# Kernel optimization log

Hardware: AMD Instinct MI355X
Metric: run time of the kernel (lower is better)

## Reference

```python
import jax, jax.numpy as jnp
import numpy as np

N, F, C, H, E, NC = 100000, 128, 64, 4, 1600000, 2
BN_EPS = 1e-5


def _bn(x, g, b):
    mu = x.mean(0)
    var = x.var(0)  # biased variance, as torch BN uses for normalization
    return (x - mu) / jnp.sqrt(var + BN_EPS) * g + b


def _gat(x, src, dst, W, a_src, a_dst, bias, heads, out_ch, concat, n):
    # x:[n,in] -> h:[n,heads,out_ch]
    h = (x @ W).reshape(n, heads, out_ch)
    e_src = (h * a_src[None]).sum(-1)  # [n,heads]
    e_dst = (h * a_dst[None]).sum(-1)
    logits = jax.nn.leaky_relu(e_src[src] + e_dst[dst], 0.2)  # [e,heads]
    m = jax.ops.segment_max(logits, dst, num_segments=n)
    m = jnp.where(jnp.isfinite(m), m, 0.0)
    ex = jnp.exp(logits - m[dst])
    denom = jax.ops.segment_sum(ex, dst, num_segments=n)
    alpha = ex / denom[dst]  # segment softmax over incoming edges
    out = jax.ops.segment_sum(alpha[:, :, None] * h[src], dst, num_segments=n)
    out = out.reshape(n, heads * out_ch) if concat else out.mean(axis=1)
    return out + bias


def _sage(x, src, dst, Wl, bl, Wr, n):
    agg = jax.ops.segment_sum(x[src], dst, num_segments=n)
    cnt = jax.ops.segment_sum(jnp.ones_like(src, dtype=x.dtype), dst, num_segments=n)
    agg = agg / jnp.maximum(cnt, 1.0)[:, None]  # mean aggregation
    return agg @ Wl + bl + x @ Wr


def setup_inputs() -> dict:
    key = jax.random.key(0)
    ks = jax.random.split(key, 24)
    def rn(k, shape, fan):
        return jax.random.normal(k, shape, jnp.float32) * (1.0 / np.sqrt(fan))
    inp = {}
    inp['x'] = jax.random.normal(ks[0], (N, F), jnp.float32)
    inp['edge_index'] = jax.random.randint(ks[1], (2, E), 0, N, jnp.int32)
    # GAT layer 1: in=F, out=C, heads=H, concat
    inp['W1g'] = rn(ks[2], (F, H * C), F)
    inp['a_src1'] = rn(ks[3], (H, C), C)
    inp['a_dst1'] = rn(ks[4], (H, C), C)
    inp['b1g'] = jnp.zeros((H * C,), jnp.float32)
    inp['bn1g_g'] = jnp.ones((H * C,), jnp.float32)
    inp['bn1g_b'] = jnp.zeros((H * C,), jnp.float32)
    # GAT layer 2: in=H*C, out=C, heads=1, no concat
    inp['W2g'] = rn(ks[5], (H * C, C), H * C)
    inp['a_src2'] = rn(ks[6], (1, C), C)
    inp['a_dst2'] = rn(ks[7], (1, C), C)
    inp['b2g'] = jnp.zeros((C,), jnp.float32)
    # SAGE layer 1
    inp['Wl1'] = rn(ks[8], (F, C), F)
    inp['bl1'] = jnp.zeros((C,), jnp.float32)
    inp['Wr1'] = rn(ks[9], (F, C), F)
    inp['bn1s_g'] = jnp.ones((C,), jnp.float32)
    inp['bn1s_b'] = jnp.zeros((C,), jnp.float32)
    # SAGE layer 2
    inp['Wl2'] = rn(ks[10], (C, C), C)
    inp['bl2'] = jnp.zeros((C,), jnp.float32)
    inp['Wr2'] = rn(ks[11], (C, C), C)
    # fusion MLP
    inp['Wf1'] = rn(ks[12], (2 * C, C), 2 * C)
    inp['bf1'] = jnp.zeros((C,), jnp.float32)
    inp['Wf2'] = rn(ks[13], (C, NC), C)
    inp['bf2'] = jnp.zeros((NC,), jnp.float32)
    return inp


def reference(x, edge_index, W1g, a_src1, a_dst1, b1g, bn1g_g, bn1g_b,
              W2g, a_src2, a_dst2, b2g, Wl1, bl1, Wr1, bn1s_g, bn1s_b,
              Wl2, bl2, Wr2, Wf1, bf1, Wf2, bf2):
    n = x.shape[0]
    src, dst = edge_index[0], edge_index[1]
    # PyG GATConv adds self-loops by default
    loop = jnp.arange(n, dtype=src.dtype)
    src_l = jnp.concatenate([src, loop])
    dst_l = jnp.concatenate([dst, loop])

    # GAT branch (dropout = identity in eval)
    g = _gat(x, src_l, dst_l, W1g, a_src1, a_dst1, b1g, H, C, True, n)
    g = jax.nn.elu(_bn(g, bn1g_g, bn1g_b))
    g = _gat(g, src_l, dst_l, W2g, a_src2, a_dst2, b2g, 1, C, False, n)

    # SAGE branch (no self-loops in SAGEConv)
    s = _sage(x, src, dst, Wl1, bl1, Wr1, n)
    s = jax.nn.relu(_bn(s, bn1s_g, bn1s_b))
    s = _sage(s, src, dst, Wl2, bl2, Wr2, n)

    h = jnp.concatenate([g, s], axis=-1)  # [n, 2C]
    h = jax.nn.relu(h @ Wf1 + bf1)
    return h @ Wf2 + bf2  # logits [n, NC]
```

## Files before the change

kernel.cpp:

```cpp
#include <hip/hip_runtime.h>
#include <math.h>


typedef unsigned short u16;
typedef u16 us4 __attribute__((ext_vector_type(4)));
typedef short s8v __attribute__((ext_vector_type(8)));
typedef float f4v __attribute__((ext_vector_type(4)));

__device__ __forceinline__ float b2f(u16 u) {
  union { unsigned int i; float f; } v; v.i = ((unsigned int)u) << 16; return v.f;
}
__device__ __forceinline__ u16 f2b(float f) {
  union { float f; unsigned int i; } v; v.f = f;
  unsigned int u = v.i;
  return (u16)((u + 0x7fffu + ((u >> 16) & 1u)) >> 16);
}

__global__ __launch_bounds__(256) void k_cast(const float* __restrict__ s, u16* __restrict__ d, int n4) {
  int i = blockIdx.x * blockDim.x + threadIdx.x;
  if (i < n4) {
    float4 v = *(reinterpret_cast<const float4*>(s) + i);
    us4 o = { f2b(v.x), f2b(v.y), f2b(v.z), f2b(v.w) };
    *(reinterpret_cast<us4*>(d) + i) = o;
  }
}

struct WcastDesc { const float* W; u16* Wt; int K; int M; };
struct WcastAll { WcastDesc d[5]; };
__global__ __launch_bounds__(256) void k_wcast_all(WcastAll a) {
  WcastDesc de = a.d[blockIdx.y];
  int n = de.K * de.M;
  int idx = blockIdx.x * blockDim.x + threadIdx.x;
  if (idx >= n) return;
  int c = idx / de.K, k = idx - c * de.K;
  de.Wt[idx] = f2b(de.W[(size_t)k * de.M + c]);
}

__global__ __launch_bounds__(256) void k_combine(const float* __restrict__ Wl2, const float* __restrict__ Wr2,
                                                 const float* __restrict__ bl2, const float* __restrict__ Wf1,
                                                 const float* __restrict__ bf1, u16* __restrict__ Wc1t,
                                                 u16* __restrict__ Wc2t, float* __restrict__ biasC) {
  int idx = blockIdx.x * 256 + threadIdx.x;
  if (idx >= 4096) return;
  int m = idx >> 6, k = idx & 63;
  float s1 = 0.f, s2 = 0.f;
  for (int j = 0; j < 64; ++j) {
    float wf = Wf1[(size_t)(64 + j) * 64 + m];
    s1 += Wl2[k * 64 + j] * wf;
    s2 += Wr2[k * 64 + j] * wf;
  }
  Wc1t[m * 64 + k] = f2b(s1);
  Wc2t[m * 64 + k] = f2b(s2);
  if (k == 0) {
    float b = bf1[m];
    for (int j = 0; j < 64; ++j) b += bl2[j] * Wf1[(size_t)(64 + j) * 64 + m];
    biasC[m] = b;
  }
}

__global__ __launch_bounds__(256) void k_deg(const int* __restrict__ ei, int* __restrict__ deg, int E) {
  int e = blockIdx.x * blockDim.x + threadIdx.x;
  if (e < E) atomicAdd(&deg[ei[E + e]], 1);
}

__global__ __launch_bounds__(256) void k_scan1(const int* __restrict__ deg, int* __restrict__ row_ptr,
                                               int* __restrict__ bsum, int n) {
  __shared__ int sh[256];
  int tid = threadIdx.x;
  int i = blockIdx.x * 256 + tid;
  int v = (i < n) ? deg[i] : 0;
  sh[tid] = v;
  __syncthreads();
  for (int off = 1; off < 256; off <<= 1) {
    int t = (tid >= off) ? sh[tid - off] : 0;
    __syncthreads();
    sh[tid] += t;
    __syncthreads();
  }
  if (i < n) row_ptr[i] = sh[tid] - v;
  if (tid == 255) bsum[blockIdx.x] = sh[255];
}

__global__ __launch_bounds__(1024) void k_scan2(int* __restrict__ bsum, int* __restrict__ total, int nb) {
  __shared__ int sh[1024];
  int tid = threadIdx.x;
  int v = (tid < nb) ? bsum[tid] : 0;
  sh[tid] = v;
  __syncthreads();
  for (int off = 1; off < 1024; off <<= 1) {
    int t = (tid >= off) ? sh[tid - off] : 0;
    __syncthreads();
    sh[tid] += t;
    __syncthreads();
  }
  if (tid < nb) bsum[tid] = sh[tid] - v;
  if (tid == 1023) *total = sh[1023];
}

__global__ __launch_bounds__(256) void k_scan3(int* __restrict__ row_ptr, const int* __restrict__ bsum, int n) {
  int i = blockIdx.x * 256 + threadIdx.x;
  if (i < n) row_ptr[i] += bsum[blockIdx.x];
}

__global__ __launch_bounds__(256) void k_scatter(const int* __restrict__ ei, const int* __restrict__ row_ptr,
                                                 int* __restrict__ cursor, int* __restrict__ csr_src, int E) {
  int e = blockIdx.x * blockDim.x + threadIdx.x;
  if (e < E) {
    int d = ei[E + e];
    int pos = row_ptr[d] + atomicAdd(&cursor[d], 1);
    csr_src[pos] = ei[e];
  }
}

struct Seg { const u16* Wt; u16* out; int ldout; const float* bias; int head; };
struct Segs6 { Seg s[6]; };
__global__ __launch_bounds__(256) void k_gemm_multi(const u16* __restrict__ A, Segs6 sg,
                                                    const float* __restrict__ a_src1, const float* __restrict__ a_dst1,
                                                    float* __restrict__ es1, float* __restrict__ ed1, int Nrows) {
  Seg seg = sg.s[blockIdx.y];
  __shared__ u16 As[64][40];
  __shared__ u16 Bs[64][40];
  int row0 = blockIdx.x * 64;
  int tid = threadIdx.x;
  int w = tid >> 6, lane = tid & 63;
  int lr = tid >> 2;
  int lseg = (tid & 3) * 8;
  f4v acc[4];
#pragma unroll
  for (int nn = 0; nn < 4; ++nn) acc[nn] = (f4v){0.f, 0.f, 0.f, 0.f};
  int ar = (w << 4) + (lane & 15);
  int ak = (lane >> 4) << 3;

  for (int k0 = 0; k0 < 128; k0 += 32) {
    __syncthreads();
    int gr = row0 + lr;
    s8v av = {};
    if (gr < Nrows) av = *reinterpret_cast<const s8v*>(A + (size_t)gr * 128 + k0 + lseg);
    *reinterpret_cast<s8v*>(&As[lr][lseg]) = av;
    s8v bv = *reinterpret_cast<const s8v*>(seg.Wt + (size_t)lr * 128 + k0 + lseg);
    *reinterpret_cast<s8v*>(&Bs[lr][lseg]) = bv;
    __syncthreads();
    s8v af = *reinterpret_cast<const s8v*>(&As[ar][ak]);
#pragma unroll
    for (int nn = 0; nn < 4; ++nn) {
      s8v bf = *reinterpret_cast<const s8v*>(&Bs[(nn << 4) + (lane & 15)][ak]);
      acc[nn] = __builtin_amdgcn_mfma_f32_16x16x32_bf16(af, bf, acc[nn], 0, 0, 0);
    }
  }
  int r0 = row0 + (w << 4) + ((lane >> 4) << 2);
  int cc = lane & 15;
#pragma unroll
  for (int nn = 0; nn < 4; ++nn) {
    int gc = (nn << 4) + cc;
    float bv = seg.bias ? seg.bias[gc] : 0.f;
#pragma unroll
    for (int j = 0; j < 4; ++j) {
      int gr = r0 + j;
      if (gr < Nrows) seg.out[(size_t)gr * seg.ldout + gc] = f2b(acc[nn][j] + bv);
    }
  }
  if (seg.head >= 0) {
    int s = seg.head;
    float pe[4] = {0.f, 0.f, 0.f, 0.f}, pd[4] = {0.f, 0.f, 0.f, 0.f};
#pragma unroll
    for (int nn = 0; nn < 4; ++nn) {
      int col = (nn << 4) + cc;
      float asv = a_src1[s * 64 + col];
      float adv = a_dst1[s * 64 + col];
#pragma unroll
      for (int j = 0; j < 4; ++j) {
        pe[j] += acc[nn][j] * asv;
        pd[j] += acc[nn][j] * adv;
      }
    }
#pragma unroll
    for (int off = 1; off < 16; off <<= 1) {
#pragma unroll
      for (int j = 0; j < 4; ++j) {
        pe[j] += __shfl_xor(pe[j], off, 64);
        pd[j] += __shfl_xor(pd[j], off, 64);
      }
    }
    if (cc == 0) {
#pragma unroll
      for (int j = 0; j < 4; ++j) {
        int gr = r0 + j;
        if (gr < Nrows) {
          es1[(size_t)gr * 4 + s] = pe[j];
          ed1[(size_t)gr * 4 + s] = pd[j];
        }
      }
    }
  }
}

__global__ __launch_bounds__(256) void k_gemm_bn(const u16* __restrict__ A, const u16* __restrict__ Wt,
                                                 const float* __restrict__ sc, const float* __restrict__ sh,
                                                 const float* __restrict__ a_src2, const float* __restrict__ a_dst2,
                                                 u16* __restrict__ C, float* __restrict__ es2,
                                                 float* __restrict__ ed2, int Nrows) {
  __shared__ u16 As[64][40];
  __shared__ u16 Bs[64][40];
  int row0 = blockIdx.x * 64;
  int tid = threadIdx.x;
  int w = tid >> 6, lane = tid & 63;
  int lr = tid >> 2;
  int lseg = (tid & 3) * 8;
  f4v acc[4];
#pragma unroll
  for (int nn = 0; nn < 4; ++nn) acc[nn] = (f4v){0.f, 0.f, 0.f, 0.f};
  int ar = (w << 4) + (lane & 15);
  int ak = (lane >> 4) << 3;

  for (int k0 = 0; k0 < 256; k0 += 32) {
    __syncthreads();
    int gr = row0 + lr;
    s8v av = {};
    if (gr < Nrows) {
      av = *reinterpret_cast<const s8v*>(A + (size_t)gr * 256 + k0 + lseg);
#pragma unroll
      for (int j = 0; j < 8; ++j) {
        int c = k0 + lseg + j;
        float a = b2f((u16)av[j]) * sc[c] + sh[c];
        a = (a > 0.f) ? a : (__expf(a) - 1.f);
        av[j] = (short)f2b(a);
      }
    }
    *reinterpret_cast<s8v*>(&As[lr][lseg]) = av;
    s8v bv = *reinterpret_cast<const s8v*>(Wt + (size_t)lr * 256 + k0 + lseg);
    *reinterpret_cast<s8v*>(&Bs[lr][lseg]) = bv;
    __syncthreads();
    s8v af = *reinterpret_cast<const s8v*>(&As[ar][ak]);
#pragma unroll
    for (int nn = 0; nn < 4; ++nn) {
      s8v bf = *reinterpret_cast<const s8v*>(&Bs[(nn << 4) + (lane & 15)][ak]);
      acc[nn] = __builtin_amdgcn_mfma_f32_16x16x32_bf16(af, bf, acc[nn], 0, 0, 0);
    }
  }
  int r0 = row0 + (w << 4) + ((lane >> 4) << 2);
  int cc = lane & 15;
  float pe[4] = {0.f, 0.f, 0.f, 0.f}, pd[4] = {0.f, 0.f, 0.f, 0.f};
#pragma unroll
  for (int nn = 0; nn < 4; ++nn) {
    int gc = (nn << 4) + cc;
    float asv = a_src2[gc], adv = a_dst2[gc];
#pragma unroll
    for (int j = 0; j < 4; ++j) {
      float hv = acc[nn][j];
      pe[j] += hv * asv;
      pd[j] += hv * adv;
      int gr = r0 + j;
      if (gr < Nrows) C[(size_t)gr * 64 + gc] = f2b(hv);
    }
  }
#pragma unroll
  for (int off = 1; off < 16; off <<= 1) {
#pragma unroll
    for (int j = 0; j < 4; ++j) {
      pe[j] += __shfl_xor(pe[j], off, 64);
      pd[j] += __shfl_xor(pd[j], off, 64);
    }
  }
  if (cc == 0) {
#pragma unroll
    for (int j = 0; j < 4; ++j) {
      int gr = r0 + j;
      if (gr < Nrows) { es2[gr] = pe[j]; ed2[gr] = pd[j]; }
    }
  }
}

__global__ __launch_bounds__(256) void k_gat_stats4(const float* __restrict__ es, const float* __restrict__ ed,
                                                    const int* __restrict__ row_ptr, const int* __restrict__ csr,
                                                    float* __restrict__ alphaE, float* __restrict__ alphaS, int n) {
  int wid = (blockIdx.x * blockDim.x + threadIdx.x) >> 6;
  int lane = threadIdx.x & 63;
  if (wid >= n) return;
  int start = row_ptr[wid];
  int deg = row_ptr[wid + 1] - start;
  int h = lane & 3, esl = lane >> 2;
  float edst = ed[(size_t)wid * 4 + h];

  float m = -1e30f, s = 0.f;
  for (int e = esl; e < deg + 1; e += 16) {
    int sn = (e < deg) ? csr[start + e] : wid;
    float v = es[(size_t)sn * 4 + h] + edst;
    v = (v >= 0.f) ? v : 0.2f * v;
    if (v > m) { s = s * __expf(m - v) + 1.f; m = v; }
    else s += __expf(v - m);
  }
#pragma unroll
  for (int off = 4; off < 64; off <<= 1) {
    float mo = __shfl_xor(m, off, 64);
    float so = __shfl_xor(s, off, 64);
    float M = fmaxf(m, mo);
    s = s * __expf(m - M) + so * __expf(mo - M);
    m = M;
  }
  float invS = 1.f / s;
  for (int e = esl; e < deg + 1; e += 16) {
    int sn = (e < deg) ? csr[start + e] : wid;
    float v = es[(size_t)sn * 4 + h] + edst;
    v = (v >= 0.f) ? v : 0.2f * v;
    float a = __expf(v - m) * invS;
    if (e < deg) alphaE[(size_t)(start + e) * 4 + h] = a;
    else alphaS[(size_t)wid * 4 + h] = a;
  }
}

__global__ __launch_bounds__(256) void k_gat_stats1(const float* __restrict__ es, const float* __restrict__ ed,
                                                    const int* __restrict__ row_ptr, const int* __restrict__ csr,
                                                    float* __restrict__ alphaE, float* __restrict__ alphaS, int n) {
  int wid = (blockIdx.x * blockDim.x + threadIdx.x) >> 6;
  int lane = threadIdx.x & 63;
  if (wid >= n) return;
  int start = row_ptr[wid];
  int deg = row_ptr[wid + 1] - start;
  float edst = ed[wid];
  float m = -1e30f, s = 0.f;
  for (int e = lane; e < deg + 1; e += 64) {
    int sn = (e < deg) ? csr[start + e] : wid;
    float v = es[sn] + edst;
    v = (v >= 0.f) ? v : 0.2f * v;
    if (v > m) { s = s * __expf(m - v) + 1.f; m = v; }
    else s += __expf(v - m);
  }
#pragma unroll
  for (int off = 1; off < 64; off <<= 1) {
    float mo = __shfl_xor(m, off, 64);
    float so = __shfl_xor(s, off, 64);
    float M = fmaxf(m, mo);
    s = s * __expf(m - M) + so * __expf(mo - M);
    m = M;
  }
  float invS = 1.f / s;
  for (int e = lane; e < deg + 1; e += 64) {
    int sn = (e < deg) ? csr[start + e] : wid;
    float v = es[sn] + edst;
    v = (v >= 0.f) ? v : 0.2f * v;
    float a = __expf(v - m) * invS;
    if (e < deg) alphaE[start + e] = a;
    else alphaS[wid] = a;
  }
}

template <int H, int C>
__global__ __launch_bounds__(256) void k_gat_agg2(const u16* __restrict__ h, const float* __restrict__ alphaE,
                                                  const float* __restrict__ alphaS, const int* __restrict__ row_ptr,
                                                  const int* __restrict__ csr, const float* __restrict__ bias,
                                                  u16* __restrict__ out, int n) {
  constexpr int HC = H * C;
  constexpr int VW = HC / 64;
  int wid = (blockIdx.x * blockDim.x + threadIdx.x) >> 6;
  int lane = threadIdx.x & 63;
  if (wid >= n) return;
  int start = row_ptr[wid];
  int deg = row_ptr[wid + 1] - start;
  int hl = (lane * VW) / C;

  float acc[VW];
  {
    float aS = alphaS[(size_t)wid * H + hl];
    if constexpr (VW == 4) {
      us4 hv = *(reinterpret_cast<const us4*>(h + (size_t)wid * HC) + lane);
#pragma unroll
      for (int j = 0; j < 4; ++j) acc[j] = aS * b2f(hv[j]);
    } else {
      acc[0] = aS * b2f(h[(size_t)wid * HC + lane]);
    }
  }

  int e = 0;
  for (; e + 4 <= deg; e += 4) {
    int sn[4];
    float al[4];
#pragma unroll
    for (int i = 0; i < 4; ++i) {
      sn[i] = csr[start + e + i];
      al[i] = alphaE[(size_t)(start + e + i) * H + hl];
    }
#pragma unroll
    for (int i = 0; i < 4; ++i) {
      if constexpr (VW == 4) {
        us4 hv = *(reinterpret_cast<const us4*>(h + (size_t)sn[i] * HC) + lane);
#pragma unroll
        for (int j = 0; j < 4; ++j) acc[j] += al[i] * b2f(hv[j]);
      } else {
        acc[0] += al[i] * b2f(h[(size_t)sn[i] * HC + lane]);
      }
    }
  }
  for (; e < deg; ++e) {
    int sn = csr[start + e];
    float al = alphaE[(size_t)(start + e) * H + hl];
    if constexpr (VW == 4) {
      us4 hv = *(reinterpret_cast<const us4*>(h + (size_t)sn * HC) + lane);
#pragma unroll
      for (int j = 0; j < 4; ++j) acc[j] += al * b2f(hv[j]);
    } else {
      acc[0] += al * b2f(h[(size_t)sn * HC + lane]);
    }
  }

  int c0 = lane * VW;
#pragma unroll
  for (int j = 0; j < VW; ++j) out[(size_t)wid * HC + c0 + j] = f2b(acc[j] + bias[c0 + j]);
}

__global__ __launch_bounds__(256) void k_sage_agg64(const u16* __restrict__ x, const int* __restrict__ row_ptr,
                                                    const int* __restrict__ csr, const u16* __restrict__ Cin,
                                                    const float* __restrict__ sc, const float* __restrict__ sh,
                                                    u16* __restrict__ agg, int n) {
  int wid = (blockIdx.x * blockDim.x + threadIdx.x) >> 6;
  int lane = threadIdx.x & 63;
  if (wid >= n) return;
  int start = row_ptr[wid];
  int deg = row_ptr[wid + 1] - start;
  bool bn = sc != nullptr;
  float scv = 1.f, shv = 0.f;
  if (bn) { scv = sc[lane]; shv = sh[lane]; }
  float acc = 0.f;
  int e = 0;
  for (; e + 4 <= deg; e += 4) {
    int sn[4];
#pragma unroll
    for (int i = 0; i < 4; ++i) sn[i] = csr[start + e + i];
#pragma unroll
    for (int i = 0; i < 4; ++i) {
      float v = b2f(x[(size_t)sn[i] * 64 + lane]);
      if (bn) v = fmaxf(v * scv + shv, 0.f);
      acc += v;
    }
  }
  for (; e < deg; ++e) {
    float v = b2f(x[(size_t)csr[start + e] * 64 + lane]);
    if (bn) v = fmaxf(v * scv + shv, 0.f);
    acc += v;
  }
  float inv = 1.f / fmaxf((float)deg, 1.f);
  float base = Cin ? b2f(Cin[(size_t)wid * 64 + lane]) : 0.f;
  agg[(size_t)wid * 64 + lane] = f2b(acc * inv + base);
}

template <int CH>
__global__ __launch_bounds__(256) void k_bn_stats(const u16* __restrict__ x, float* __restrict__ stats, int n) {
  constexpr int RPB = 256 / CH;
  int tid = threadIdx.x;
  int c = tid % CH;
  int rsub = tid / CH;
  float s = 0.f, q = 0.f;
  for (int r = blockIdx.x * RPB + rsub; r < n; r += gridDim.x * RPB) {
    float v = b2f(x[(size_t)r * CH + c]);
    s += v;
    q += v * v;
  }
  __shared__ float ls[256], lq[256];
  ls[tid] = s; lq[tid] = q;
  __syncthreads();
  if (tid < CH) {
#pragma unroll
    for (int i = 1; i < RPB; ++i) { s += ls[tid + i * CH]; q += lq[tid + i * CH]; }
    atomicAdd(&stats[c], s);
    atomicAdd(&stats[CH + c], q);
  }
}

__global__ __launch_bounds__(256) void k_bn_final2(const float* __restrict__ statsG, const float* __restrict__ statsS,
                                                   const float* __restrict__ gG, const float* __restrict__ bG,
                                                   const float* __restrict__ gS, const float* __restrict__ bS,
                                                   float* __restrict__ scG, float* __restrict__ shG,
                                                   float* __restrict__ scS, float* __restrict__ shS, int n) {
  int c = threadIdx.x;
  float invn = 1.f / (float)n;
  {
    float mu = statsG[c] * invn;
    float var = statsG[256 + c] * invn - mu * mu;
    float rs = rsqrtf(var + 1e-5f) * gG[c];
    scG[c] = rs;
    shG[c] = bG[c] - mu * rs;
  }
  if (c < 64) {
    float mu = statsS[c] * invn;
    float var = statsS[64 + c] * invn - mu * mu;
    float rs = rsqrtf(var + 1e-5f) * gS[c];
    scS[c] = rs;
    shS[c] = bS[c] - mu * rs;
  }
}

__global__ __launch_bounds__(256) void k_gemm_final(const u16* __restrict__ A1, const u16* __restrict__ W1,
                                                    const u16* __restrict__ A2, const u16* __restrict__ W2,
                                                    const u16* __restrict__ A3, const u16* __restrict__ W3,
                                                    const float* __restrict__ scS, const float* __restrict__ shS,
                                                    const float* __restrict__ biasC, const float* __restrict__ Wf2,
                                                    const float* __restrict__ bf2, float* __restrict__ out,
                                                    int Nrows) {
  __shared__ u16 As[64][40];
  __shared__ u16 Bs[64][40];
  int row0 = blockIdx.x * 64;
  int tid = threadIdx.x;
  int w = tid >> 6, lane = tid & 63;
  int lr = tid >> 2;
  int lseg = (tid & 3) * 8;
  f4v acc[4];
#pragma unroll
  for (int nn = 0; nn < 4; ++nn) acc[nn] = (f4v){0.f, 0.f, 0.f, 0.f};
  int ar = (w << 4) + (lane & 15);
  int ak = (lane >> 4) << 3;

  const u16* Aarr[3] = {A1, A2, A3};
  const u16* Warr[3] = {W1, W2, W3};
#pragma unroll
  for (int ph = 0; ph < 3; ++ph) {
    const u16* A = Aarr[ph];
    const u16* Wt = Warr[ph];
#pragma unroll
    for (int k0 = 0; k0 < 64; k0 += 32) {
      __syncthreads();
      int gr = row0 + lr;
      s8v av = {};
      if (gr < Nrows) {
        av = *reinterpret_cast<const s8v*>(A + (size_t)gr * 64 + k0 + lseg);
        if (ph == 2) {
#pragma unroll
          for (int j = 0; j < 8; ++j) {
            int c = k0 + lseg + j;
            float a = fmaxf(b2f((u16)av[j]) * scS[c] + shS[c], 0.f);
            av[j] = (short)f2b(a);
          }
        }
      }
      *reinterpret_cast<s8v*>(&As[lr][lseg]) = av;
      s8v bv = *reinterpret_cast<const s8v*>(Wt + (size_t)lr * 64 + k0 + lseg);
      *reinterpret_cast<s8v*>(&Bs[lr][lseg]) = bv;
      __syncthreads();
      s8v af = *reinterpret_cast<const s8v*>(&As[ar][ak]);
#pragma unroll
      for (int nn = 0; nn < 4; ++nn) {
        s8v bf = *reinterpret_cast<const s8v*>(&Bs[(nn << 4) + (lane & 15)][ak]);
        acc[nn] = __builtin_amdgcn_mfma_f32_16x16x32_bf16(af, bf, acc[nn], 0, 0, 0);
      }
    }
  }

  int r0 = row0 + (w << 4) + ((lane >> 4) << 2);
  int cc = lane & 15;
  float p0[4] = {0.f, 0.f, 0.f, 0.f}, p1[4] = {0.f, 0.f, 0.f, 0.f};
#pragma unroll
  for (int nn = 0; nn < 4; ++nn) {
    int col = (nn << 4) + cc;
    float bC = biasC[col];
    float w0 = Wf2[col * 2 + 0], w1 = Wf2[col * 2 + 1];
#pragma unroll
    for (int j = 0; j < 4; ++j) {
      float f = fmaxf(acc[nn][j] + bC, 0.f);
      p0[j] += f * w0;
      p1[j] += f * w1;
    }
  }
#pragma unroll
  for (int off = 1; off < 16; off <<= 1) {
#pragma unroll
    for (int j = 0; j < 4; ++j) {
      p0[j] += __shfl_xor(p0[j], off, 64);
      p1[j] += __shfl_xor(p1[j], off, 64);
    }
  }
  if (cc == 0) {
    float b0 = bf2[0], b1 = bf2[1];
#pragma unroll
    for (int j = 0; j < 4; ++j) {
      int gr = r0 + j;
      if (gr < Nrows) {
        out[(size_t)gr * 2 + 0] = p0[j] + b0;
        out[(size_t)gr * 2 + 1] = p1[j] + b1;
      }
    }
  }
}

extern "C" void kernel_launch(void* const* d_in, const int* in_sizes, int n_in,
                              void* d_out, int out_size, void* d_ws, size_t ws_size,
                              hipStream_t stream) {
  const float* x      = (const float*)d_in[0];
  const int*   ei     = (const int*)d_in[1];
  const float* W1g    = (const float*)d_in[2];
  const float* a_src1 = (const float*)d_in[3];
  const float* a_dst1 = (const float*)d_in[4];
  const float* b1g    = (const float*)d_in[5];
  const float* bn1g_g = (const float*)d_in[6];
  const float* bn1g_b = (const float*)d_in[7];
  const float* W2g    = (const float*)d_in[8];
  const float* a_src2 = (const float*)d_in[9];
  const float* a_dst2 = (const float*)d_in[10];
  const float* b2g    = (const float*)d_in[11];
  const float* Wl1    = (const float*)d_in[12];
  const float* bl1    = (const float*)d_in[13];
  const float* Wr1    = (const float*)d_in[14];
  const float* bn1s_g = (const float*)d_in[15];
  const float* bn1s_b = (const float*)d_in[16];
  const float* Wl2    = (const float*)d_in[17];
  const float* bl2    = (const float*)d_in[18];
  const float* Wr2    = (const float*)d_in[19];
  const float* Wf1    = (const float*)d_in[20];
  const float* bf1    = (const float*)d_in[21];
  const float* Wf2    = (const float*)d_in[22];
  const float* bf2    = (const float*)d_in[23];

  const int N = in_sizes[0] / 128;
  const int E = in_sizes[1] / 2;

  char* ws = (char*)d_ws;
  size_t off = 0;
  auto alloc = [&](size_t bytes) -> void* {
    size_t o = (off + 255) & ~(size_t)255;
    off = o + bytes;
    return (void*)(ws + o);
  };

  u16* xb    = (u16*)alloc((size_t)N * 128 * 2);
  u16* h1b   = (u16*)alloc((size_t)N * 256 * 2);
  u16* gb    = (u16*)alloc((size_t)N * 256 * 2);
  u16* h2b   = (u16*)alloc((size_t)N * 64 * 2);
  u16* g2b   = (u16*)alloc((size_t)N * 64 * 2);
  u16* xlb   = (u16*)alloc((size_t)N * 64 * 2);
  u16* xrb   = (u16*)alloc((size_t)N * 64 * 2);
  u16* s1b   = (u16*)alloc((size_t)N * 64 * 2);
  float* es1 = (float*)alloc((size_t)N * 4 * 4);
  float* ed1 = (float*)alloc((size_t)N * 4 * 4);
  float* es2 = (float*)alloc((size_t)N * 4);
  float* ed2 = (float*)alloc((size_t)N * 4);
  float* alphaE = (float*)alloc((size_t)E * 4 * 4);
  float* alphaS = (float*)alloc((size_t)N * 4 * 4);
  int* deg     = (int*)alloc((size_t)N * 2 * 4);
  int* cursor  = deg + N;
  int* row_ptr = (int*)alloc((size_t)(N + 1) * 4);
  int* bsum    = (int*)alloc(1024 * 4);
  int* csr     = (int*)alloc((size_t)E * 4);
  float* statsG = (float*)alloc((512 + 128) * 4);
  float* statsS = statsG + 512;
  float* scg   = (float*)alloc(256 * 4);
  float* shg   = (float*)alloc(256 * 4);
  float* scs   = (float*)alloc(64 * 4);
  float* shs   = (float*)alloc(64 * 4);
  float* biasC = (float*)alloc(64 * 4);
  u16* W1t  = (u16*)alloc(256 * 128 * 2);
  u16* W2t  = (u16*)alloc(64 * 256 * 2);
  u16* Wl1t = (u16*)alloc(64 * 128 * 2);
  u16* Wr1t = (u16*)alloc(64 * 128 * 2);
  u16* Wf1at= (u16*)alloc(64 * 64 * 2);
  u16* Wc1t = (u16*)alloc(64 * 64 * 2);
  u16* Wc2t = (u16*)alloc(64 * 64 * 2);
  u16* sagg2b = h1b;

  const int tb = 256;
  const int nwb = (N + 3) / 4;
  const int nsb = (N + 255) / 256;
  const int gx = (N + 63) / 64;

  hipMemsetAsync(deg, 0, (size_t)N * 2 * 4, stream);
  hipMemsetAsync(statsG, 0, (512 + 128) * 4, stream);
  k_deg<<<(E + tb - 1) / tb, tb, 0, stream>>>(ei, deg, E);
  k_scan1<<<nsb, 256, 0, stream>>>(deg, row_ptr, bsum, N);
  k_scan2<<<1, 1024, 0, stream>>>(bsum, row_ptr + N, nsb);
  k_scan3<<<nsb, 256, 0, stream>>>(row_ptr, bsum, N);
  k_scatter<<<(E + tb - 1) / tb, tb, 0, stream>>>(ei, row_ptr, cursor, csr, E);

  k_cast<<<((N * 128 / 4) + tb - 1) / tb, tb, 0, stream>>>(x, xb, N * 128 / 4);
  WcastAll wa;
  wa.d[0] = { W1g, W1t, 128, 256 };
  wa.d[1] = { W2g, W2t, 256, 64 };
  wa.d[2] = { Wl1, Wl1t, 128, 64 };
  wa.d[3] = { Wr1, Wr1t, 128, 64 };
  wa.d[4] = { Wf1, Wf1at, 64, 64 };
  dim3 wgrid((128 * 256 + tb - 1) / tb, 5);
  k_wcast_all<<<wgrid, tb, 0, stream>>>(wa);
  k_combine<<<16, 256, 0, stream>>>(Wl2, Wr2, bl2, Wf1, bf1, Wc1t, Wc2t, biasC);

  Segs6 sg;
  sg.s[0] = { W1t,             h1b + 0,   256, nullptr, 0 };
  sg.s[1] = { W1t + 64 * 128,  h1b + 64,  256, nullptr, 1 };
  sg.s[2] = { W1t + 128 * 128, h1b + 128, 256, nullptr, 2 };
  sg.s[3] = { W1t + 192 * 128, h1b + 192, 256, nullptr, 3 };
  sg.s[4] = { Wl1t,            xlb, 64, nullptr, -1 };
  sg.s[5] = { Wr1t,            xrb, 64, bl1,     -1 };
  k_gemm_multi<<<dim3(gx, 6), 256, 0, stream>>>(xb, sg, a_src1, a_dst1, es1, ed1, N);

  k_gat_stats4<<<nwb, 256, 0, stream>>>(es1, ed1, row_ptr, csr, alphaE, alphaS, N);
  k_gat_agg2<4, 64><<<nwb, 256, 0, stream>>>(h1b, alphaE, alphaS, row_ptr, csr, b1g, gb, N);
  k_bn_stats<256><<<256, 256, 0, stream>>>(gb, statsG, N);

  k_sage_agg64<<<nwb, 256, 0, stream>>>(xlb, row_ptr, csr, xrb, nullptr, nullptr, s1b, N);
  k_bn_stats<64><<<256, 256, 0, stream>>>(s1b, statsS, N);
  k_bn_final2<<<1, 256, 0, stream>>>(statsG, statsS, bn1g_g, bn1g_b, bn1s_g, bn1s_b,
                                     scg, shg, scs, shs, N);

  k_gemm_bn<<<gx, 256, 0, stream>>>(gb, W2t, scg, shg, a_src2, a_dst2, h2b, es2, ed2, N);
  k_gat_stats1<<<nwb, 256, 0, stream>>>(es2, ed2, row_ptr, csr, alphaE, alphaS, N);
  k_gat_agg2<1, 64><<<nwb, 256, 0, stream>>>(h2b, alphaE, alphaS, row_ptr, csr, b2g, g2b, N);

  k_sage_agg64<<<nwb, 256, 0, stream>>>(s1b, row_ptr, csr, nullptr, scs, shs, sagg2b, N);

  k_gemm_final<<<gx, 256, 0, stream>>>(g2b, Wf1at, sagg2b, Wc1t, s1b, Wc2t,
                                       scs, shs, biasC, Wf2, bf2, (float*)d_out, N);
}
```

Before: 798.4 us.

## Fuse GAT and SAGE aggregations, BN stats, weight prep, and input cast

Merges the GAT and SAGE neighbour aggregations of each layer into one kernel, so the CSR indices and row pointers are read once per node for both branches. Merges the two BN statistics kernels into one launch and the weight-cast and weight-combine kernels into one. Drops the separate bf16 cast of x: the first GEMM now reads fp32 x and converts it while loading. This cuts kernel launches and the extra traffic of the cast buffer, at the cost of more registers per aggregation kernel and the GEMM re-reading fp32 x once for each of its 6 column segments.

```diff
diff --git a/kernel.cpp b/kernel.cpp
--- a/kernel.cpp
+++ b/kernel.cpp
@@ -16,45 +16,38 @@
   return (u16)((u + 0x7fffu + ((u >> 16) & 1u)) >> 16);
 }
 
-__global__ __launch_bounds__(256) void k_cast(const float* __restrict__ s, u16* __restrict__ d, int n4) {
-  int i = blockIdx.x * blockDim.x + threadIdx.x;
-  if (i < n4) {
-    float4 v = *(reinterpret_cast<const float4*>(s) + i);
-    us4 o = { f2b(v.x), f2b(v.y), f2b(v.z), f2b(v.w) };
-    *(reinterpret_cast<us4*>(d) + i) = o;
-  }
-}
-
 struct WcastDesc { const float* W; u16* Wt; int K; int M; };
-struct WcastAll { WcastDesc d[5]; };
-__global__ __launch_bounds__(256) void k_wcast_all(WcastAll a) {
-  WcastDesc de = a.d[blockIdx.y];
-  int n = de.K * de.M;
-  int idx = blockIdx.x * blockDim.x + threadIdx.x;
-  if (idx >= n) return;
-  int c = idx / de.K, k = idx - c * de.K;
-  de.Wt[idx] = f2b(de.W[(size_t)k * de.M + c]);
-}
-
-__global__ __launch_bounds__(256) void k_combine(const float* __restrict__ Wl2, const float* __restrict__ Wr2,
-                                                 const float* __restrict__ bl2, const float* __restrict__ Wf1,
-                                                 const float* __restrict__ bf1, u16* __restrict__ Wc1t,
-                                                 u16* __restrict__ Wc2t, float* __restrict__ biasC) {
+struct WPrep {
+  WcastDesc d[5];
+  const float *Wl2, *Wr2, *bl2, *Wf1, *bf1;
+  u16 *Wc1t, *Wc2t;
+  float* biasC;
+};
+__global__ __launch_bounds__(256) void k_wprep(WPrep a) {
+  int y = blockIdx.y;
   int idx = blockIdx.x * 256 + threadIdx.x;
-  if (idx >= 4096) return;
-  int m = idx >> 6, k = idx & 63;
-  float s1 = 0.f, s2 = 0.f;
-  for (int j = 0; j < 64; ++j) {
-    float wf = Wf1[(size_t)(64 + j) * 64 + m];
-    s1 += Wl2[k * 64 + j] * wf;
-    s2 += Wr2[k * 64 + j] * wf;
-  }
-  Wc1t[m * 64 + k] = f2b(s1);
-  Wc2t[m * 64 + k] = f2b(s2);
-  if (k == 0) {
-    float b = bf1[m];
-    for (int j = 0; j < 64; ++j) b += bl2[j] * Wf1[(size_t)(64 + j) * 64 + m];
-    biasC[m] = b;
+  if (y < 5) {
+    WcastDesc de = a.d[y];
+    int n = de.K * de.M;
+    if (idx >= n) return;
+    int c = idx / de.K, k = idx - c * de.K;
+    de.Wt[idx] = f2b(de.W[(size_t)k * de.M + c]);
+  } else {
+    if (idx >= 4096) return;
+    int m = idx >> 6, k = idx & 63;
+    float s1 = 0.f, s2 = 0.f;
+    for (int j = 0; j < 64; ++j) {
+      float wf = a.Wf1[(size_t)(64 + j) * 64 + m];
+      s1 += a.Wl2[k * 64 + j] * wf;
+      s2 += a.Wr2[k * 64 + j] * wf;
+    }
+    a.Wc1t[m * 64 + k] = f2b(s1);
+    a.Wc2t[m * 64 + k] = f2b(s2);
+    if (k == 0) {
+      float b = a.bf1[m];
+      for (int j = 0; j < 64; ++j) b += a.bl2[j] * a.Wf1[(size_t)(64 + j) * 64 + m];
+      a.biasC[m] = b;
+    }
   }
 }
 
@@ -114,7 +107,7 @@
 
 struct Seg { const u16* Wt; u16* out; int ldout; const float* bias; int head; };
 struct Segs6 { Seg s[6]; };
-__global__ __launch_bounds__(256) void k_gemm_multi(const u16* __restrict__ A, Segs6 sg,
+__global__ __launch_bounds__(256) void k_gemm_multi(const float* __restrict__ X, Segs6 sg,
                                                     const float* __restrict__ a_src1, const float* __restrict__ a_dst1,
                                                     float* __restrict__ es1, float* __restrict__ ed1, int Nrows) {
   Seg seg = sg.s[blockIdx.y];
@@ -135,7 +128,12 @@
     __syncthreads();
     int gr = row0 + lr;
     s8v av = {};
-    if (gr < Nrows) av = *reinterpret_cast<const s8v*>(A + (size_t)gr * 128 + k0 + lseg);
+    if (gr < Nrows) {
+      float4 lo = *reinterpret_cast<const float4*>(X + (size_t)gr * 128 + k0 + lseg);
+      float4 hi = *reinterpret_cast<const float4*>(X + (size_t)gr * 128 + k0 + lseg + 4);
+      av[0] = (short)f2b(lo.x); av[1] = (short)f2b(lo.y); av[2] = (short)f2b(lo.z); av[3] = (short)f2b(lo.w);
+      av[4] = (short)f2b(hi.x); av[5] = (short)f2b(hi.y); av[6] = (short)f2b(hi.z); av[7] = (short)f2b(hi.w);
+    }
     *reinterpret_cast<s8v*>(&As[lr][lseg]) = av;
     s8v bv = *reinterpret_cast<const s8v*>(seg.Wt + (size_t)lr * 128 + k0 + lseg);
     *reinterpret_cast<s8v*>(&Bs[lr][lseg]) = bv;
@@ -344,30 +342,25 @@
   }
 }
 
-template <int H, int C>
-__global__ __launch_bounds__(256) void k_gat_agg2(const u16* __restrict__ h, const float* __restrict__ alphaE,
-                                                  const float* __restrict__ alphaS, const int* __restrict__ row_ptr,
-                                                  const int* __restrict__ csr, const float* __restrict__ bias,
-                                                  u16* __restrict__ out, int n) {
-  constexpr int HC = H * C;
-  constexpr int VW = HC / 64;
+__global__ __launch_bounds__(256) void k_agg_gs1(const u16* __restrict__ h1, const u16* __restrict__ xl,
+                                                 const u16* __restrict__ xr, const float* __restrict__ alphaE,
+                                                 const float* __restrict__ alphaS, const int* __restrict__ row_ptr,
+                                                 const int* __restrict__ csr, const float* __restrict__ b1g,
+                                                 u16* __restrict__ gb, u16* __restrict__ s1, int n) {
   int wid = (blockIdx.x * blockDim.x + threadIdx.x) >> 6;
   int lane = threadIdx.x & 63;
   if (wid >= n) return;
   int start = row_ptr[wid];
   int deg = row_ptr[wid + 1] - start;
-  int hl = (lane * VW) / C;
-
-  float acc[VW];
+  int hl = lane >> 4;
+
+  float accG[4];
+  float accS = 0.f;
   {
-    float aS = alphaS[(size_t)wid * H + hl];
-    if constexpr (VW == 4) {
-      us4 hv = *(reinterpret_cast<const us4*>(h + (size_t)wid * HC) + lane);
-#pragma unroll
-      for (int j = 0; j < 4; ++j) acc[j] = aS * b2f(hv[j]);
-    } else {
-      acc[0] = aS * b2f(h[(size_t)wid * HC + lane]);
-    }
+    float aS = alphaS[(size_t)wid * 4 + hl];
+    us4 hv = *(reinterpret_cast<const us4*>(h1 + (size_t)wid * 256) + lane);
+#pragma unroll
+    for (int j = 0; j < 4; ++j) accG[j] = aS * b2f(hv[j]);
   }
 
   int e = 0;
@@ -377,91 +370,106 @@
 #pragma unroll
     for (int i = 0; i < 4; ++i) {
       sn[i] = csr[start + e + i];
-      al[i] = alphaE[(size_t)(start + e + i) * H + hl];
+      al[i] = alphaE[(size_t)(start + e + i) * 4 + hl];
     }
 #pragma unroll
     for (int i = 0; i < 4; ++i) {
-      if constexpr (VW == 4) {
-        us4 hv = *(reinterpret_cast<const us4*>(h + (size_t)sn[i] * HC) + lane);
-#pragma unroll
-        for (int j = 0; j < 4; ++j) acc[j] += al[i] * b2f(hv[j]);
-      } else {
-        acc[0] += al[i] * b2f(h[(size_t)sn[i] * HC + lane]);
-      }
+      us4 hv = *(reinterpret_cast<const us4*>(h1 + (size_t)sn[i] * 256) + lane);
+#pragma unroll
+      for (int j = 0; j < 4; ++j) accG[j] += al[i] * b2f(hv[j]);
+      accS += b2f(xl[(size_t)sn[i] * 64 + lane]);
     }
   }
   for (; e < deg; ++e) {
     int sn = csr[start + e];
-    float al = alphaE[(size_t)(start + e) * H + hl];
-    if constexpr (VW == 4) {
-      us4 hv = *(reinterpret_cast<const us4*>(h + (size_t)sn * HC) + lane);
-#pragma unroll
-      for (int j = 0; j < 4; ++j) acc[j] += al * b2f(hv[j]);
-    } else {
-      acc[0] += al * b2f(h[(size_t)sn * HC + lane]);
-    }
-  }
-
-  int c0 = lane * VW;
-#pragma unroll
-  for (int j = 0; j < VW; ++j) out[(size_t)wid * HC + c0 + j] = f2b(acc[j] + bias[c0 + j]);
-}
-
-__global__ __launch_bounds__(256) void k_sage_agg64(const u16* __restrict__ x, const int* __restrict__ row_ptr,
-                                                    const int* __restrict__ csr, const u16* __restrict__ Cin,
-                                                    const float* __restrict__ sc, const float* __restrict__ sh,
-                                                    u16* __restrict__ agg, int n) {
+    float al = alphaE[(size_t)(start + e) * 4 + hl];
+    us4 hv = *(reinterpret_cast<const us4*>(h1 + (size_t)sn * 256) + lane);
+#pragma unroll
+    for (int j = 0; j < 4; ++j) accG[j] += al * b2f(hv[j]);
+    accS += b2f(xl[(size_t)sn * 64 + lane]);
+  }
+
+  int c0 = lane * 4;
+#pragma unroll
+  for (int j = 0; j < 4; ++j) gb[(size_t)wid * 256 + c0 + j] = f2b(accG[j] + b1g[c0 + j]);
+  float inv = 1.f / fmaxf((float)deg, 1.f);
+  s1[(size_t)wid * 64 + lane] = f2b(accS * inv + b2f(xr[(size_t)wid * 64 + lane]));
+}
+
+__global__ __launch_bounds__(256) void k_agg_gs2(const u16* __restrict__ h2, const u16* __restrict__ s1,
+                                                 const float* __restrict__ alphaE, const float* __restrict__ alphaS,
+                                                 const int* __restrict__ row_ptr, const int* __restrict__ csr,
+                                                 const float* __restrict__ b2g, const float* __restrict__ scs,
+                                                 const float* __restrict__ shs, u16* __restrict__ g2,
+                                                 u16* __restrict__ sagg2, int n) {
   int wid = (blockIdx.x * blockDim.x + threadIdx.x) >> 6;
   int lane = threadIdx.x & 63;
   if (wid >= n) return;
   int start = row_ptr[wid];
   int deg = row_ptr[wid + 1] - start;
-  bool bn = sc != nullptr;
-  float scv = 1.f, shv = 0.f;
-  if (bn) { scv = sc[lane]; shv = sh[lane]; }
-  float acc = 0.f;
+  float scv = scs[lane], shv = shs[lane];
+
+  float accG = alphaS[wid] * b2f(h2[(size_t)wid * 64 + lane]);
+  float accS = 0.f;
   int e = 0;
   for (; e + 4 <= deg; e += 4) {
     int sn[4];
-#pragma unroll
-    for (int i = 0; i < 4; ++i) sn[i] = csr[start + e + i];
+    float al[4];
 #pragma unroll
     for (int i = 0; i < 4; ++i) {
-      float v = b2f(x[(size_t)sn[i] * 64 + lane]);
-      if (bn) v = fmaxf(v * scv + shv, 0.f);
-      acc += v;
+      sn[i] = csr[start + e + i];
+      al[i] = alphaE[start + e + i];
+    }
+#pragma unroll
+    for (int i = 0; i < 4; ++i) {
+      accG += al[i] * b2f(h2[(size_t)sn[i] * 64 + lane]);
+      accS += fmaxf(b2f(s1[(size_t)sn[i] * 64 + lane]) * scv + shv, 0.f);
     }
   }
   for (; e < deg; ++e) {
-    float v = b2f(x[(size_t)csr[start + e] * 64 + lane]);
-    if (bn) v = fmaxf(v * scv + shv, 0.f);
-    acc += v;
-  }
+    int sn = csr[start + e];
+    accG += alphaE[start + e] * b2f(h2[(size_t)sn * 64 + lane]);
+    accS += fmaxf(b2f(s1[(size_t)sn * 64 + lane]) * scv + shv, 0.f);
+  }
+
+  g2[(size_t)wid * 64 + lane] = f2b(accG + b2g[lane]);
   float inv = 1.f / fmaxf((float)deg, 1.f);
-  float base = Cin ? b2f(Cin[(size_t)wid * 64 + lane]) : 0.f;
-  agg[(size_t)wid * 64 + lane] = f2b(acc * inv + base);
-}
-
-template <int CH>
-__global__ __launch_bounds__(256) void k_bn_stats(const u16* __restrict__ x, float* __restrict__ stats, int n) {
-  constexpr int RPB = 256 / CH;
+  sagg2[(size_t)wid * 64 + lane] = f2b(accS * inv);
+}
+
+__global__ __launch_bounds__(256) void k_bn_stats_both(const u16* __restrict__ gb, const u16* __restrict__ s1,
+                                                       float* __restrict__ statsG, float* __restrict__ statsS,
+                                                       int n) {
   int tid = threadIdx.x;
-  int c = tid % CH;
-  int rsub = tid / CH;
-  float s = 0.f, q = 0.f;
-  for (int r = blockIdx.x * RPB + rsub; r < n; r += gridDim.x * RPB) {
-    float v = b2f(x[(size_t)r * CH + c]);
-    s += v;
-    q += v * v;
-  }
   __shared__ float ls[256], lq[256];
-  ls[tid] = s; lq[tid] = q;
-  __syncthreads();
-  if (tid < CH) {
-#pragma unroll
-    for (int i = 1; i < RPB; ++i) { s += ls[tid + i * CH]; q += lq[tid + i * CH]; }
-    atomicAdd(&stats[c], s);
-    atomicAdd(&stats[CH + c], q);
+  if (blockIdx.x < 256) {
+    int c = tid;
+    float s = 0.f, q = 0.f;
+    for (int r = blockIdx.x; r < n; r += 256) {
+      float v = b2f(gb[(size_t)r * 256 + c]);
+      s += v;
+      q += v * v;
+    }
+    atomicAdd(&statsG[c], s);
+    atomicAdd(&statsG[256 + c], q);
+  } else {
+    int bx = blockIdx.x - 256;
+    int c = tid & 63;
+    int rsub = tid >> 6;
+    float s = 0.f, q = 0.f;
+    for (int r = bx * 4 + rsub; r < n; r += 256 * 4) {
+      float v = b2f(s1[(size_t)r * 64 + c]);
+      s += v;
+      q += v * v;
+    }
+    ls[tid] = s; lq[tid] = q;
+    __syncthreads();
+    if (tid < 64) {
+#pragma unroll
+      for (int i = 1; i < 4; ++i) { s += ls[tid + i * 64]; q += lq[tid + i * 64]; }
+      atomicAdd(&statsS[c], s);
+      atomicAdd(&statsS[64 + c], q);
+    }
   }
 }
 
@@ -618,7 +626,6 @@
     return (void*)(ws + o);
   };
 
-  u16* xb    = (u16*)alloc((size_t)N * 128 * 2);
   u16* h1b   = (u16*)alloc((size_t)N * 256 * 2);
   u16* gb    = (u16*)alloc((size_t)N * 256 * 2);
   u16* h2b   = (u16*)alloc((size_t)N * 64 * 2);
@@ -666,16 +673,16 @@
   k_scan3<<<nsb, 256, 0, stream>>>(row_ptr, bsum, N);
   k_scatter<<<(E + tb - 1) / tb, tb, 0, stream>>>(ei, row_ptr, cursor, csr, E);
 
-  k_cast<<<((N * 128 / 4) + tb - 1) / tb, tb, 0, stream>>>(x, xb, N * 128 / 4);
-  WcastAll wa;
-  wa.d[0] = { W1g, W1t, 128, 256 };
-  wa.d[1] = { W2g, W2t, 256, 64 };
-  wa.d[2] = { Wl1, Wl1t, 128, 64 };
-  wa.d[3] = { Wr1, Wr1t, 128, 64 };
-  wa.d[4] = { Wf1, Wf1at, 64, 64 };
-  dim3 wgrid((128 * 256 + tb - 1) / tb, 5);
-  k_wcast_all<<<wgrid, tb, 0, stream>>>(wa);
-  k_combine<<<16, 256, 0, stream>>>(Wl2, Wr2, bl2, Wf1, bf1, Wc1t, Wc2t, biasC);
+  WPrep wp;
+  wp.d[0] = { W1g, W1t, 128, 256 };
+  wp.d[1] = { W2g, W2t, 256, 64 };
+  wp.d[2] = { Wl1, Wl1t, 128, 64 };
+  wp.d[3] = { Wr1, Wr1t, 128, 64 };
+  wp.d[4] = { Wf1, Wf1at, 64, 64 };
+  wp.Wl2 = Wl2; wp.Wr2 = Wr2; wp.bl2 = bl2; wp.Wf1 = Wf1; wp.bf1 = bf1;
+  wp.Wc1t = Wc1t; wp.Wc2t = Wc2t; wp.biasC = biasC;
+  dim3 wgrid((128 * 256 + tb - 1) / tb, 6);
+  k_wprep<<<wgrid, tb, 0, stream>>>(wp);
 
   Segs6 sg;
   sg.s[0] = { W1t,             h1b + 0,   256, nullptr, 0 };
@@ -684,22 +691,18 @@
   sg.s[3] = { W1t + 192 * 128, h1b + 192, 256, nullptr, 3 };
   sg.s[4] = { Wl1t,            xlb, 64, nullptr, -1 };
   sg.s[5] = { Wr1t,            xrb, 64, bl1,     -1 };
-  k_gemm_multi<<<dim3(gx, 6), 256, 0, stream>>>(xb, sg, a_src1, a_dst1, es1, ed1, N);
+  k_gemm_multi<<<dim3(gx, 6), 256, 0, stream>>>(x, sg, a_src1, a_dst1, es1, ed1, N);
 
   k_gat_stats4<<<nwb, 256, 0, stream>>>(es1, ed1, row_ptr, csr, alphaE, alphaS, N);
-  k_gat_agg2<4, 64><<<nwb, 256, 0, stream>>>(h1b, alphaE, alphaS, row_ptr, csr, b1g, gb, N);
-  k_bn_stats<256><<<256, 256, 0, stream>>>(gb, statsG, N);
-
-  k_sage_agg64<<<nwb, 256, 0, stream>>>(xlb, row_ptr, csr, xrb, nullptr, nullptr, s1b, N);
-  k_bn_stats<64><<<256, 256, 0, stream>>>(s1b, statsS, N);
+  k_agg_gs1<<<nwb, 256, 0, stream>>>(h1b, xlb, xrb, alphaE, alphaS, row_ptr, csr, b1g, gb, s1b, N);
+  k_bn_stats_both<<<512, 256, 0, stream>>>(gb, s1b, statsG, statsS, N);
   k_bn_final2<<<1, 256, 0, stream>>>(statsG, statsS, bn1g_g, bn1g_b, bn1s_g, bn1s_b,
                                      scg, shg, scs, shs, N);
 
   k_gemm_bn<<<gx, 256, 0, stream>>>(gb, W2t, scg, shg, a_src2, a_dst2, h2b, es2, ed2, N);
   k_gat_stats1<<<nwb, 256, 0, stream>>>(es2, ed2, row_ptr, csr, alphaE, alphaS, N);
-  k_gat_agg2<1, 64><<<nwb, 256, 0, stream>>>(h2b, alphaE, alphaS, row_ptr, csr, b2g, g2b, N);
-
-  k_sage_agg64<<<nwb, 256, 0, stream>>>(s1b, row_ptr, csr, nullptr, scs, shs, sagg2b, N);
+  k_agg_gs2<<<nwb, 256, 0, stream>>>(h2b, s1b, alphaE, alphaS, row_ptr, csr, b2g, scs, shs,
+                                     g2b, sagg2b, N);
 
   k_gemm_final<<<gx, 256, 0, stream>>>(g2b, Wf1at, sagg2b, Wc1t, s1b, Wc2t,
                                        scs, shs, biasC, Wf2, bf2, (float*)d_out, N);
```

Result: faster. 687.4 us (-13.9%).
